# Performance work log

Measured on AMD Instinct MI355X. Metric: run time of the kernel, lower is better.

Reference implementation:

```python
import jax, jax.numpy as jnp
import numpy as np

M = 16          # num_particles
EPS = 0.006


def setup_inputs() -> dict:
    key = jax.random.key(0)
    k1, k2, k3, k4 = jax.random.split(key, 4)
    B, P, O = 131072, 16, 4  # batch, pred_horizon, obs_horizon
    return {
        "ys_t": jax.random.normal(k1, (B, P, O), dtype=jnp.float32),
        "ys_r_stop": jax.random.normal(k2, (B, P, O), dtype=jnp.float32),
        "w_scale": jax.random.uniform(k3, (B,), dtype=jnp.float32),
        "time_weights": jax.random.uniform(k4, (B,), dtype=jnp.float32),
    }


def _laplace(a, b, ws, D):
    # a,b: [G, M, D]; ws: [G, M] (scale indexed by j, the first particle index)
    d = jnp.linalg.norm(a[:, :, None, :] - b[:, None, :, :], axis=-1)  # [G, M, M]
    d = jnp.maximum(d, EPS)
    return jnp.exp(-ws[:, :, None] * d / D)


def reference(ys_t, ys_r_stop, w_scale, time_weights):
    B = ys_t.shape[0]
    G = B // M
    x = ys_t.reshape(G, M, -1)        # [G, M, D]
    y = ys_r_stop.reshape(G, M, -1)   # [G, M, D]
    D = x.shape[-1]                   # pred_horizon * obs_horizon (dim_normalize)
    ws = w_scale.reshape(G, M)
    tw = time_weights.reshape(G, M)[:, 0]  # [G]
    terms = _laplace(x, x, ws, D) + _laplace(y, y, ws, D) - 2.0 * _laplace(x, y, ws, D)
    group_loss = terms.sum(axis=(1, 2)) * tw / (M * M)  # [G]
    return group_loss.sum() / G
```

## Files before the change

kernel.cpp:

```cpp
#include <hip/hip_runtime.h>


#define EPS_D 0.006f

#define ROT(v, O) __int_as_float(__builtin_amdgcn_update_dpp(              \
        0, __float_as_int(v), 0x120 + (O), 0xF, 0xF, false))

__device__ __forceinline__ float red4(float p) {
    p += __shfl_xor(p, 16, 64);
    p += __shfl_xor(p, 32, 64);
    return p;
}

#define FULL_O(O, W) {                                                     \
    float pxx = 0.f, pyy = 0.f, pxy = 0.f;                                 \
    _Pragma("unroll")                                                      \
    for (int d = 0; d < 16; ++d) {                                         \
        float tx = ROT(xd[d], O) - xd[d];         \
        float tz = ROT(yd[d], O) - xd[d];         \
        float ty = tz + dl[d];                                 \
        pxx = fmaf(tx, tx, pxx);                                           \
        pyy = fmaf(ty, ty, pyy);                                           \
        pxy = fmaf(tz, tz, pxy);                                           \
    }                                                                      \
    pxx = red4(pxx);  pyy = red4(pyy);  pxy = red4(pxy);                   \
    const float s_k = ROT(s_j, O);                                         \
    const float ddx = fmaxf(sqrtf(pxx), EPS_D);                            \
    const float ddy = fmaxf(sqrtf(pyy), EPS_D);                            \
    const float ddz = fmaxf(sqrtf(pxy), EPS_D);                            \
    acc += (W) * (__expf(-s_j * ddx) + __expf(-s_k * ddx));                \
    acc += (W) * (__expf(-s_j * ddy) + __expf(-s_k * ddy));                \
    acc -= 2.0f * __expf(-s_j * ddz); }

#define XY_O(O) {                                                          \
    float pxy = 0.f;                                                       \
    _Pragma("unroll")                                                      \
    for (int d = 0; d < 16; ++d) {                                         \
        float tz = ROT(yd[d], O) - xd[d];                                  \
        pxy = fmaf(tz, tz, pxy);                                           \
    }                                                                      \
    pxy = red4(pxy);                                                       \
    acc -= 2.0f * __expf(-s_j * fmaxf(sqrtf(pxy), EPS_D)); }

__global__ __launch_bounds__(256, 4)
void imm_loss_kernel(const float* __restrict__ ys_t,
                     const float* __restrict__ ys_r,
                     const float* __restrict__ w_scale,
                     const float* __restrict__ time_w,
                     float* __restrict__ partials)
{
    const int tid  = threadIdx.x;
    const int lane = tid & 63;
    const int wave = tid >> 6;
    const int q    = lane >> 4;
    const int j    = lane & 15;
    const int g    = blockIdx.x * 4 + wave;

    const size_t base = (size_t)g * 1024 + j * 64 + q * 16;
    const float4* xp = reinterpret_cast<const float4*>(ys_t + base);
    const float4* yp = reinterpret_cast<const float4*>(ys_r + base);

    float xd[16], yd[16], dl[16];
    #pragma unroll
    for (int t = 0; t < 4; ++t) {
        float4 v = xp[t];
        xd[4*t+0] = v.x; xd[4*t+1] = v.y; xd[4*t+2] = v.z; xd[4*t+3] = v.w;
    }
    #pragma unroll
    for (int t = 0; t < 4; ++t) {
        float4 v = yp[t];
        yd[4*t+0] = v.x; yd[4*t+1] = v.y; yd[4*t+2] = v.z; yd[4*t+3] = v.w;
    }
    #pragma unroll
    for (int d = 0; d < 16; ++d) dl[d] = xd[d] - yd[d];

    const float s_j = w_scale[g * 16 + j] * (1.0f / 64.0f);
    const float tw  = time_w[g * 16];

    float acc = 2.0f * __expf(-s_j * EPS_D);

    {
        float p0 = 0.f;
        #pragma unroll
        for (int d = 0; d < 16; ++d) p0 = fmaf(dl[d], dl[d], p0);
        p0 = red4(p0);
        acc -= 2.0f * __expf(-s_j * fmaxf(sqrtf(p0), EPS_D));
    }

    FULL_O(1, 1.0f)
    FULL_O(2, 1.0f)
    FULL_O(3, 1.0f)
    FULL_O(4, 1.0f)
    FULL_O(5, 1.0f)
    FULL_O(6, 1.0f)
    FULL_O(7, 1.0f)
    FULL_O(8, 0.5f)
    XY_O(9)
    XY_O(10)
    XY_O(11)
    XY_O(12)
    XY_O(13)
    XY_O(14)
    XY_O(15)

    float val = acc * tw;
    #pragma unroll
    for (int off = 32; off; off >>= 1)
        val += __shfl_xor(val, off, 64);

    __shared__ float smem[4];
    if (lane == 0) smem[wave] = val;
    __syncthreads();
    if (tid == 0)
        partials[blockIdx.x] = smem[0] + smem[1] + smem[2] + smem[3];
}

__global__ void imm_reduce_kernel(const float* __restrict__ part, int n,
                                  float inv_scale, float* __restrict__ out)
{
    const int tid = threadIdx.x;
    float v = 0.f;
    for (int i = tid; i < n; i += 256) v += part[i];
    #pragma unroll
    for (int off = 32; off; off >>= 1) v += __shfl_xor(v, off, 64);
    __shared__ float s[4];
    if ((tid & 63) == 0) s[tid >> 6] = v;
    __syncthreads();
    if (tid == 0) out[0] = (s[0] + s[1] + s[2] + s[3]) * inv_scale;
}

extern "C" void kernel_launch(void* const* d_in, const int* in_sizes, int n_in,
                              void* d_out, int out_size, void* d_ws, size_t ws_size,
                              hipStream_t stream)
{
    const float* ys_t = (const float*)d_in[0];
    const float* ys_r = (const float*)d_in[1];
    const float* wsc  = (const float*)d_in[2];
    const float* twp  = (const float*)d_in[3];
    float* out      = (float*)d_out;
    float* partials = (float*)d_ws;

    const int B = in_sizes[2];
    const int G = B / 16;
    const int blocks = G / 4;

    imm_loss_kernel<<<blocks, 256, 0, stream>>>(ys_t, ys_r, wsc, twp, partials);

    const float inv_scale = 1.0f / (4.0f * 256.0f * (float)G);
    imm_reduce_kernel<<<1, 256, 0, stream>>>(partials, blocks, inv_scale, out);
}
```

Before: 118.5 us.

## Interchange loops to stream dimensions and accumulate all offsets per dimension

The loop order is inverted: instead of holding all 16 x, y and diff values per lane and looping over rotation offsets, each loaded dimension value is consumed immediately by updating 32 per-offset partial sums. Reductions, sqrt and exp then run in a separate epilogue. This drops the 48-float input arrays in favour of 32 accumulators, aiming to lower register pressure and let the loads overlap with compute. The cost is more live accumulators in flight during the loads, and the epilogue's cross-lane reductions are now bunched together.

```diff
diff --git a/kernel.cpp b/kernel.cpp
--- a/kernel.cpp
+++ b/kernel.cpp
@@ -12,35 +12,26 @@
     return p;
 }
 
-#define FULL_O(O, W) {                                                     \
-    float pxx = 0.f, pyy = 0.f, pxy = 0.f;                                 \
-    _Pragma("unroll")                                                      \
-    for (int d = 0; d < 16; ++d) {                                         \
-        float tx = ROT(xd[d], O) - xd[d];         \
-        float tz = ROT(yd[d], O) - xd[d];         \
-        float ty = tz + dl[d];                                 \
-        pxx = fmaf(tx, tx, pxx);                                           \
-        pyy = fmaf(ty, ty, pyy);                                           \
-        pxy = fmaf(tz, tz, pxy);                                           \
-    }                                                                      \
-    pxx = red4(pxx);  pyy = red4(pyy);  pxy = red4(pxy);                   \
-    const float s_k = ROT(s_j, O);                                         \
-    const float ddx = fmaxf(sqrtf(pxx), EPS_D);                            \
-    const float ddy = fmaxf(sqrtf(pyy), EPS_D);                            \
-    const float ddz = fmaxf(sqrtf(pxy), EPS_D);                            \
-    acc += (W) * (__expf(-s_j * ddx) + __expf(-s_k * ddx));                \
-    acc += (W) * (__expf(-s_j * ddy) + __expf(-s_k * ddy));                \
-    acc -= 2.0f * __expf(-s_j * ddz); }
+#define UPD_FULL(O) {                                                      \
+    float tx = ROT(xv, O) - xv;        \
+    float tz = ROT(yv, O) - xv;                                \
+    float ty = tz + dl;                                        \
+    fxx[(O)-1] = fmaf(tx, tx, fxx[(O)-1]);                                 \
+    fyy[(O)-1] = fmaf(ty, ty, fyy[(O)-1]);                                 \
+    fxy[(O)-1] = fmaf(tz, tz, fxy[(O)-1]); }
 
-#define XY_O(O) {                                                          \
-    float pxy = 0.f;                                                       \
-    _Pragma("unroll")                                                      \
-    for (int d = 0; d < 16; ++d) {                                         \
-        float tz = ROT(yd[d], O) - xd[d];                                  \
-        pxy = fmaf(tz, tz, pxy);                                           \
-    }                                                                      \
-    pxy = red4(pxy);                                                       \
-    acc -= 2.0f * __expf(-s_j * fmaxf(sqrtf(pxy), EPS_D)); }
+#define UPD_XY(O) {                                                        \
+    float tz = ROT(yv, O) - xv;                                            \
+    gxy[(O)-8] = fmaf(tz, tz, gxy[(O)-8]); }
+
+#define DIM_STEP(XV, YV) {                                                 \
+    const float xv = (XV), yv = (YV);                                      \
+    const float dl = xv - yv;                                              \
+    gxy[0] = fmaf(dl, dl, gxy[0]);               \
+    UPD_FULL(1) UPD_FULL(2) UPD_FULL(3) UPD_FULL(4)                        \
+    UPD_FULL(5) UPD_FULL(6) UPD_FULL(7) UPD_FULL(8)                        \
+    UPD_XY(9) UPD_XY(10) UPD_XY(11) UPD_XY(12)                             \
+    UPD_XY(13) UPD_XY(14) UPD_XY(15) }
 
 __global__ __launch_bounds__(256, 4)
 void imm_loss_kernel(const float* __restrict__ ys_t,
@@ -60,19 +51,19 @@
     const float4* xp = reinterpret_cast<const float4*>(ys_t + base);
     const float4* yp = reinterpret_cast<const float4*>(ys_r + base);
 
-    float xd[16], yd[16], dl[16];
+    float fxx[8], fyy[8], fxy[8], gxy[8];
+    #pragma unroll
+    for (int i = 0; i < 8; ++i) { fxx[i] = 0.f; fyy[i] = 0.f; fxy[i] = 0.f; gxy[i] = 0.f; }
+
     #pragma unroll
     for (int t = 0; t < 4; ++t) {
-        float4 v = xp[t];
-        xd[4*t+0] = v.x; xd[4*t+1] = v.y; xd[4*t+2] = v.z; xd[4*t+3] = v.w;
+        float4 xv4 = xp[t];
+        float4 yv4 = yp[t];
+        DIM_STEP(xv4.x, yv4.x)
+        DIM_STEP(xv4.y, yv4.y)
+        DIM_STEP(xv4.z, yv4.z)
+        DIM_STEP(xv4.w, yv4.w)
     }
-    #pragma unroll
-    for (int t = 0; t < 4; ++t) {
-        float4 v = yp[t];
-        yd[4*t+0] = v.x; yd[4*t+1] = v.y; yd[4*t+2] = v.z; yd[4*t+3] = v.w;
-    }
-    #pragma unroll
-    for (int d = 0; d < 16; ++d) dl[d] = xd[d] - yd[d];
 
     const float s_j = w_scale[g * 16 + j] * (1.0f / 64.0f);
     const float tw  = time_w[g * 16];
@@ -80,28 +71,30 @@
     float acc = 2.0f * __expf(-s_j * EPS_D);
 
     {
-        float p0 = 0.f;
-        #pragma unroll
-        for (int d = 0; d < 16; ++d) p0 = fmaf(dl[d], dl[d], p0);
-        p0 = red4(p0);
+        float p0 = red4(gxy[0]);
         acc -= 2.0f * __expf(-s_j * fmaxf(sqrtf(p0), EPS_D));
     }
 
-    FULL_O(1, 1.0f)
-    FULL_O(2, 1.0f)
-    FULL_O(3, 1.0f)
-    FULL_O(4, 1.0f)
-    FULL_O(5, 1.0f)
-    FULL_O(6, 1.0f)
-    FULL_O(7, 1.0f)
-    FULL_O(8, 0.5f)
-    XY_O(9)
-    XY_O(10)
-    XY_O(11)
-    XY_O(12)
-    XY_O(13)
-    XY_O(14)
-    XY_O(15)
+#define EPI_FULL(O, W) {                                                   \
+        float pxx = red4(fxx[(O)-1]);                                      \
+        float pyy = red4(fyy[(O)-1]);                                      \
+        float pxy = red4(fxy[(O)-1]);                                      \
+        const float s_k = ROT(s_j, O);                                     \
+        const float ddx = fmaxf(sqrtf(pxx), EPS_D);                        \
+        const float ddy = fmaxf(sqrtf(pyy), EPS_D);                        \
+        const float ddz = fmaxf(sqrtf(pxy), EPS_D);                        \
+        acc += (W) * (__expf(-s_j * ddx) + __expf(-s_k * ddx));            \
+        acc += (W) * (__expf(-s_j * ddy) + __expf(-s_k * ddy));            \
+        acc -= 2.0f * __expf(-s_j * ddz); }
+
+#define EPI_XY(O) {                                                        \
+        float pxy = red4(gxy[(O)-8]);                                      \
+        acc -= 2.0f * __expf(-s_j * fmaxf(sqrtf(pxy), EPS_D)); }
+
+    EPI_FULL(1, 1.0f) EPI_FULL(2, 1.0f) EPI_FULL(3, 1.0f) EPI_FULL(4, 1.0f)
+    EPI_FULL(5, 1.0f) EPI_FULL(6, 1.0f) EPI_FULL(7, 1.0f) EPI_FULL(8, 0.5f)
+    EPI_XY(9) EPI_XY(10) EPI_XY(11) EPI_XY(12)
+    EPI_XY(13) EPI_XY(14) EPI_XY(15)
 
     float val = acc * tw;
     #pragma unroll
```

New measurement: 119.5 us. No clear change (+0.9%).
